# Performance work log

Hardware: AMD Instinct MI355X
Metric: run time of the kernel (lower is better)

## Reference

```python
import jax, jax.numpy as jnp
import numpy as np

N_NODES = 65536  # total nodes across batch (64 graphs x 1024 nodes)


def _gcn_conv(x, W, b, src, dst, norm, num_nodes):
    # PyG GCNConv: h = x @ W; out_i = sum_{j->i} norm_ij * h_j + b
    h = x @ W  # [N, out_dim]
    msg = h[src] * norm[:, None]  # [E+N, out_dim]
    out = jax.ops.segment_sum(msg, dst, num_segments=num_nodes)
    return out + b


def _add_self_loops_and_norm(edge_index, num_nodes):
    # add self loops, compute symmetric normalization deg^-1/2 * deg^-1/2
    loops = jnp.arange(num_nodes, dtype=edge_index.dtype)
    src = jnp.concatenate([edge_index[0], loops])
    dst = jnp.concatenate([edge_index[1], loops])
    deg = jax.ops.segment_sum(jnp.ones_like(dst, dtype=jnp.float32), dst,
                              num_segments=num_nodes)
    dinv = jnp.where(deg > 0, jax.lax.rsqrt(jnp.maximum(deg, 1.0)), 0.0)
    norm = dinv[src] * dinv[dst]
    return src, dst, norm


def setup_inputs() -> dict:
    key = jax.random.key(0)
    k1, k2, k3, k4, k5 = jax.random.split(key, 5)
    num_features, latent = 128, 16
    x = jax.random.normal(k1, (N_NODES, num_features), dtype=jnp.float32)
    edge_index = jax.random.randint(k2, (2, 2097152), 0, N_NODES, dtype=jnp.int64)
    # Glorot-style params for conv1 (128->16) and conv2 (16->1)
    W1 = jax.random.normal(k3, (num_features, latent), dtype=jnp.float32) / np.sqrt(num_features)
    b1 = jnp.zeros((latent,), dtype=jnp.float32)
    W2 = jax.random.normal(k4, (latent, 1), dtype=jnp.float32) / np.sqrt(latent)
    b2 = jnp.zeros((1,), dtype=jnp.float32)
    return {"x": x, "W1": W1, "b1": b1, "W2": W2, "b2": b2,
            "edge_index": edge_index, "batch": 64}


def reference(x, W1, b1, W2, b2, edge_index, batch):
    num_nodes = x.shape[0]
    src, dst, norm = _add_self_loops_and_norm(edge_index, num_nodes)
    h = _gcn_conv(x, W1, b1, src, dst, norm, num_nodes)  # [N, 16]
    h = jax.nn.relu(h)
    h = _gcn_conv(h, W2, b2, src, dst, norm, num_nodes)  # [N, 1]
    return h.reshape(batch, -1)  # [batch, nodes_per_graph]
```

## Files before the change

kernel.cpp:

```cpp
#include <hip/hip_runtime.h>

#define FEAT 128
#define LAT  16
#define NB   256
#define NPB  256
#define CAP  10240
#define PBLK 512
#define PCHK 4096
#define CAPB 64
#define CAPBKT (PBLK * CAPB)

__global__ __launch_bounds__(512) void k_part(const int* __restrict__ src,
        const int* __restrict__ dst, int E, int* __restrict__ cnt,
        int* __restrict__ ebuf) {
    __shared__ int lcur[NB];
    int t = threadIdx.x;
    if (t < NB) lcur[t] = 0;
    __syncthreads();
    int e0 = blockIdx.x * PCHK;
    int e1 = min(e0 + PCHK, E);
    int c = max(e1 - e0, 0);
    int cb = blockIdx.x * CAPB;
    const int4* d4 = (const int4*)(dst + e0);
    const int4* s4 = (const int4*)(src + e0);
    int nq = c >> 2;
    for (int q = t; q < nq; q += 512) {
        int4 dv = d4[q];
        int4 sv = s4[q];
        int b0 = ((unsigned)dv.x) >> 8, b1 = ((unsigned)dv.y) >> 8;
        int b2 = ((unsigned)dv.z) >> 8, b3 = ((unsigned)dv.w) >> 8;
        int p0 = atomicAdd(&lcur[b0], 1);
        int p1 = atomicAdd(&lcur[b1], 1);
        int p2 = atomicAdd(&lcur[b2], 1);
        int p3 = atomicAdd(&lcur[b3], 1);
        if (p0 < CAPB) ebuf[b0 * CAPBKT + cb + p0] = (sv.x << 16) | dv.x;
        if (p1 < CAPB) ebuf[b1 * CAPBKT + cb + p1] = (sv.y << 16) | dv.y;
        if (p2 < CAPB) ebuf[b2 * CAPBKT + cb + p2] = (sv.z << 16) | dv.z;
        if (p3 < CAPB) ebuf[b3 * CAPBKT + cb + p3] = (sv.w << 16) | dv.w;
    }
    for (int e = (nq << 2) + t; e < c; e += 512) {
        int d = dst[e0 + e], s = src[e0 + e];
        int b = ((unsigned)d) >> 8;
        int p = atomicAdd(&lcur[b], 1);
        if (p < CAPB) ebuf[b * CAPBKT + cb + p] = (s << 16) | d;
    }
    __syncthreads();
    if (t < NB) cnt[(blockIdx.x << 8) | t] = min(lcur[t], CAPB);
}

__global__ __launch_bounds__(512) void k_csr(const int* __restrict__ ebuf,
        const int* __restrict__ cnt, const float* __restrict__ x,
        const float* __restrict__ W1, int* __restrict__ rsd,
        unsigned short* __restrict__ csr, float* __restrict__ hs) {
    __shared__ int stage[CAP];
    __shared__ int ccnt[PBLK];
    __shared__ int cpref[PBLK];
    __shared__ int h[NPB];
    __shared__ int sc[NPB];
    __shared__ int cur[NPB];
    __shared__ int total;
    int t = threadIdx.x;
    int b = blockIdx.x;
    ccnt[t] = cnt[(t << 8) | b];
    if (t < NPB) h[t] = 0;
    __syncthreads();
    cpref[t] = ccnt[t];
    __syncthreads();
    for (int off = 1; off < PBLK; off <<= 1) {
        int v = (t >= off) ? cpref[t - off] : 0;
        __syncthreads();
        cpref[t] += v;
        __syncthreads();
    }
    if (t == PBLK - 1) total = min(cpref[t], CAP);
    int excl = cpref[t] - ccnt[t];
    __syncthreads();
    cpref[t] = excl;
    __syncthreads();
    int lane = t & 7;
    int crel = t >> 3;
    for (int cg = 0; cg < PBLK; cg += 64) {
        int ch = cg + crel;
        int cc = ccnt[ch];
        int gbase = b * CAPBKT + ch * CAPB;
        int sbase = cpref[ch];
        for (int i = lane; i < cc; i += 8) {
            int v = ebuf[gbase + i];
            if (sbase + i < CAP) {
                stage[sbase + i] = v;
                atomicAdd(&h[v & 255], 1);
            }
        }
    }
    __syncthreads();
    int cntall = total;
    if (t < NPB) sc[t] = h[t];
    __syncthreads();
    for (int off = 1; off < NPB; off <<= 1) {
        int v = (t >= off && t < NPB) ? sc[t - off] : 0;
        __syncthreads();
        if (t < NPB) sc[t] += v;
        __syncthreads();
    }
    if (t < NPB) {
        int excl2 = t ? sc[t - 1] : 0;
        int node = b * NPB + t;
        rsd[node] = ((b * CAP + excl2) << 8) | min(h[t], 255);
        cur[t] = b * CAP + excl2;
    }
    __syncthreads();
    int e = t;
    for (; e + 1536 < cntall; e += 2048) {
        int v0 = stage[e], v1 = stage[e + 512], v2 = stage[e + 1024], v3 = stage[e + 1536];
        int p0 = atomicAdd(&cur[v0 & 255], 1);
        int p1 = atomicAdd(&cur[v1 & 255], 1);
        int p2 = atomicAdd(&cur[v2 & 255], 1);
        int p3 = atomicAdd(&cur[v3 & 255], 1);
        csr[p0] = (unsigned)v0 >> 16;
        csr[p1] = (unsigned)v1 >> 16;
        csr[p2] = (unsigned)v2 >> 16;
        csr[p3] = (unsigned)v3 >> 16;
    }
    for (; e < cntall; e += 512) {
        int v = stage[e];
        int pos = atomicAdd(&cur[v & 255], 1);
        csr[pos] = (unsigned)v >> 16;
    }
    __syncthreads();
    float* w = (float*)stage;
    for (int i = t; i < FEAT * LAT; i += 512) {
        int k = i >> 4, j = i & 15;
        w[(k << 4) + j + ((k >> 5) << 2)] = W1[i];
    }
    __syncthreads();
    int q = t & 3;
    int qofs = q << 2;
#pragma unroll
    for (int pass = 0; pass < 2; ++pass) {
        int nl = pass * 128 + (t >> 2);
        int node = b * NPB + nl;
        float acc[LAT];
#pragma unroll
        for (int j = 0; j < LAT; ++j) acc[j] = 0.f;
        const float4* xr = (const float4*)(x + (size_t)node * FEAT + q * 32);
#pragma unroll
        for (int k4 = 0; k4 < 8; ++k4) {
            float4 xv = xr[k4];
            int kb = (q * 32 + k4 * 4) * LAT + qofs;
#pragma unroll
            for (int j = 0; j < LAT; ++j) {
                acc[j] += xv.x * w[kb + 0 * LAT + j]
                        + xv.y * w[kb + 1 * LAT + j]
                        + xv.z * w[kb + 2 * LAT + j]
                        + xv.w * w[kb + 3 * LAT + j];
            }
        }
#pragma unroll
        for (int j = 0; j < LAT; ++j) {
            acc[j] += __shfl_xor(acc[j], 1, 4);
            acc[j] += __shfl_xor(acc[j], 2, 4);
        }
        float dv = rsqrtf((float)(h[nl] + 1));
        float4 ov;
        if (q == 0)      ov = make_float4(acc[0],  acc[1],  acc[2],  acc[3]);
        else if (q == 1) ov = make_float4(acc[4],  acc[5],  acc[6],  acc[7]);
        else if (q == 2) ov = make_float4(acc[8],  acc[9],  acc[10], acc[11]);
        else             ov = make_float4(acc[12], acc[13], acc[14], acc[15]);
        ov.x *= dv; ov.y *= dv; ov.z *= dv; ov.w *= dv;
        ((float4*)(hs + (size_t)node * LAT))[q] = ov;
    }
}

__global__ void k_conv1(const float* __restrict__ hs, const int* __restrict__ rsd,
                        const unsigned short* __restrict__ csr,
                        const float* __restrict__ b1, const float* __restrict__ W2,
                        float* __restrict__ g, int n) {
    int t = threadIdx.x;
    int lane16 = t & 15;
    int jq = t & 3;
    int es = (t >> 2) & 3;
    int node = blockIdx.x * 16 + (t >> 4);
    int rd = rsd[node];
    int s0 = rd >> 8, deg = rd & 255;
    int s1 = s0 + deg;
    const float4* hs4 = (const float4*)hs;
    float4 acc = make_float4(0.f, 0.f, 0.f, 0.f);
    if (es == 0) acc = hs4[(size_t)node * 4 + jq];
    int e = s0 + es;
    for (; e + 28 < s1; e += 32) {
        int i0 = csr[e],      i1 = csr[e + 4],  i2 = csr[e + 8],  i3 = csr[e + 12];
        int i4 = csr[e + 16], i5 = csr[e + 20], i6 = csr[e + 24], i7 = csr[e + 28];
        float4 a0 = hs4[(size_t)i0 * 4 + jq];
        float4 a1 = hs4[(size_t)i1 * 4 + jq];
        float4 a2 = hs4[(size_t)i2 * 4 + jq];
        float4 a3 = hs4[(size_t)i3 * 4 + jq];
        float4 a4 = hs4[(size_t)i4 * 4 + jq];
        float4 a5 = hs4[(size_t)i5 * 4 + jq];
        float4 a6 = hs4[(size_t)i6 * 4 + jq];
        float4 a7 = hs4[(size_t)i7 * 4 + jq];
        acc.x += ((a0.x + a1.x) + (a2.x + a3.x)) + ((a4.x + a5.x) + (a6.x + a7.x));
        acc.y += ((a0.y + a1.y) + (a2.y + a3.y)) + ((a4.y + a5.y) + (a6.y + a7.y));
        acc.z += ((a0.z + a1.z) + (a2.z + a3.z)) + ((a4.z + a5.z) + (a6.z + a7.z));
        acc.w += ((a0.w + a1.w) + (a2.w + a3.w)) + ((a4.w + a5.w) + (a6.w + a7.w));
    }
    for (; e < s1; e += 4) {
        int i = csr[e];
        float4 a = hs4[(size_t)i * 4 + jq];
        acc.x += a.x; acc.y += a.y; acc.z += a.z; acc.w += a.w;
    }
    acc.x += __shfl_xor(acc.x, 4, 16);  acc.x += __shfl_xor(acc.x, 8, 16);
    acc.y += __shfl_xor(acc.y, 4, 16);  acc.y += __shfl_xor(acc.y, 8, 16);
    acc.z += __shfl_xor(acc.z, 4, 16);  acc.z += __shfl_xor(acc.z, 8, 16);
    acc.w += __shfl_xor(acc.w, 4, 16);  acc.w += __shfl_xor(acc.w, 8, 16);
    float dv = rsqrtf((float)(deg + 1));
    float4 b1q = ((const float4*)b1)[jq];
    float4 w2q = ((const float4*)W2)[jq];
    float h0 = fmaxf(dv * acc.x + b1q.x, 0.f);
    float h1 = fmaxf(dv * acc.y + b1q.y, 0.f);
    float h2 = fmaxf(dv * acc.z + b1q.z, 0.f);
    float h3 = fmaxf(dv * acc.w + b1q.w, 0.f);
    float p = (h0 * w2q.x + h1 * w2q.y) + (h2 * w2q.z + h3 * w2q.w);
    p += __shfl_xor(p, 1, 16);
    p += __shfl_xor(p, 2, 16);
    if (lane16 == 0) g[node] = dv * p;
}

__global__ void k_conv2(const float* __restrict__ g, const int* __restrict__ rsd,
                        const unsigned short* __restrict__ csr,
                        const float* __restrict__ b2, float* __restrict__ out, int n) {
    int t = threadIdx.x;
    int q = t & 3;
    int node = blockIdx.x * 64 + (t >> 2);
    int rd = rsd[node];
    int s0 = rd >> 8, deg = rd & 255;
    int s1 = s0 + deg;
    float acc = (q == 0) ? g[node] : 0.f;
    int e = s0 + q;
    for (; e + 28 < s1; e += 32) {
        float a0 = g[csr[e]],      a1 = g[csr[e + 4]];
        float a2 = g[csr[e + 8]],  a3 = g[csr[e + 12]];
        float a4 = g[csr[e + 16]], a5 = g[csr[e + 20]];
        float a6 = g[csr[e + 24]], a7 = g[csr[e + 28]];
        acc += ((a0 + a1) + (a2 + a3)) + ((a4 + a5) + (a6 + a7));
    }
    for (; e < s1; e += 4) acc += g[csr[e]];
    acc += __shfl_xor(acc, 1, 4);
    acc += __shfl_xor(acc, 2, 4);
    if (q == 0) {
        float dv = rsqrtf((float)(deg + 1));
        out[node] = dv * acc + b2[0];
    }
}

extern "C" void kernel_launch(void* const* d_in, const int* in_sizes, int n_in,
                              void* d_out, int out_size, void* d_ws, size_t ws_size,
                              hipStream_t stream) {
    const float* x  = (const float*)d_in[0];
    const float* W1 = (const float*)d_in[1];
    const float* b1 = (const float*)d_in[2];
    const float* W2 = (const float*)d_in[3];
    const float* b2 = (const float*)d_in[4];
    const int*   ei = (const int*)d_in[5];

    int n = in_sizes[0] / FEAT;
    int E = in_sizes[5] / 2;
    const int* srcp = ei;
    const int* dstp = ei + E;

    int*   cnt  = (int*)d_ws;
    int*   rsd  = cnt + PBLK * NB;
    float* g    = (float*)(rsd + n);
    float* hs   = g + n;
    int*   ebuf = (int*)(hs + (size_t)n * LAT);
    unsigned short* csr = (unsigned short*)(ebuf + (size_t)NB * CAPBKT);

    k_part <<<PBLK, 512, 0, stream>>>(srcp, dstp, E, cnt, ebuf);
    k_csr  <<<NB, 512, 0, stream>>>(ebuf, cnt, x, W1, rsd, csr, hs);
    k_conv1<<<n / 16, 256, 0, stream>>>(hs, rsd, csr, b1, W2, g, n);
    k_conv2<<<n / 64, 256, 0, stream>>>(g, rsd, csr, b2, (float*)d_out, n);
}
```

Baseline: 76.60 us.

## Split CSR build blocks into two half-bucket blocks for more parallelism

```diff
diff --git a/kernel.cpp b/kernel.cpp
--- a/kernel.cpp
+++ b/kernel.cpp
@@ -5,6 +5,7 @@
 #define NB   256
 #define NPB  256
 #define CAP  10240
+#define HCAP 5120
 #define PBLK 512
 #define PCHK 4096
 #define CAPB 64
@@ -52,70 +53,62 @@
         const int* __restrict__ cnt, const float* __restrict__ x,
         const float* __restrict__ W1, int* __restrict__ rsd,
         unsigned short* __restrict__ csr, float* __restrict__ hs) {
-    __shared__ int stage[CAP];
+    __shared__ int stage[HCAP];
     __shared__ int ccnt[PBLK];
-    __shared__ int cpref[PBLK];
-    __shared__ int h[NPB];
-    __shared__ int sc[NPB];
-    __shared__ int cur[NPB];
-    __shared__ int total;
-    int t = threadIdx.x;
-    int b = blockIdx.x;
+    __shared__ int h[128];
+    __shared__ int sc[128];
+    __shared__ int cur[128];
+    __shared__ int hcur;
+    int t = threadIdx.x;
+    int b = blockIdx.x >> 1;
+    int hi = blockIdx.x & 1;
     ccnt[t] = cnt[(t << 8) | b];
-    if (t < NPB) h[t] = 0;
-    __syncthreads();
-    cpref[t] = ccnt[t];
-    __syncthreads();
-    for (int off = 1; off < PBLK; off <<= 1) {
-        int v = (t >= off) ? cpref[t - off] : 0;
-        __syncthreads();
-        cpref[t] += v;
-        __syncthreads();
-    }
-    if (t == PBLK - 1) total = min(cpref[t], CAP);
-    int excl = cpref[t] - ccnt[t];
-    __syncthreads();
-    cpref[t] = excl;
+    if (t < 128) h[t] = 0;
+    if (t == 0) hcur = 0;
     __syncthreads();
     int lane = t & 7;
     int crel = t >> 3;
+    int hbit = hi << 7;
     for (int cg = 0; cg < PBLK; cg += 64) {
         int ch = cg + crel;
         int cc = ccnt[ch];
         int gbase = b * CAPBKT + ch * CAPB;
-        int sbase = cpref[ch];
         for (int i = lane; i < cc; i += 8) {
             int v = ebuf[gbase + i];
-            if (sbase + i < CAP) {
-                stage[sbase + i] = v;
-                atomicAdd(&h[v & 255], 1);
+            if ((v & 128) == hbit) {
+                int p = atomicAdd(&hcur, 1);
+                if (p < HCAP) {
+                    stage[p] = v;
+                    atomicAdd(&h[v & 127], 1);
+                }
             }
         }
     }
     __syncthreads();
-    int cntall = total;
-    if (t < NPB) sc[t] = h[t];
-    __syncthreads();
-    for (int off = 1; off < NPB; off <<= 1) {
-        int v = (t >= off && t < NPB) ? sc[t - off] : 0;
+    int cntall = min(hcur, HCAP);
+    if (t < 128) sc[t] = h[t];
+    __syncthreads();
+    for (int off = 1; off < 128; off <<= 1) {
+        int v = (t >= off && t < 128) ? sc[t - off] : 0;
         __syncthreads();
-        if (t < NPB) sc[t] += v;
+        if (t < 128) sc[t] += v;
         __syncthreads();
     }
-    if (t < NPB) {
-        int excl2 = t ? sc[t - 1] : 0;
-        int node = b * NPB + t;
-        rsd[node] = ((b * CAP + excl2) << 8) | min(h[t], 255);
-        cur[t] = b * CAP + excl2;
+    int rbase = b * CAP + hi * HCAP;
+    if (t < 128) {
+        int excl = t ? sc[t - 1] : 0;
+        int node = b * NPB + hbit + t;
+        rsd[node] = ((rbase + excl) << 8) | min(h[t], 255);
+        cur[t] = rbase + excl;
     }
     __syncthreads();
     int e = t;
     for (; e + 1536 < cntall; e += 2048) {
         int v0 = stage[e], v1 = stage[e + 512], v2 = stage[e + 1024], v3 = stage[e + 1536];
-        int p0 = atomicAdd(&cur[v0 & 255], 1);
-        int p1 = atomicAdd(&cur[v1 & 255], 1);
-        int p2 = atomicAdd(&cur[v2 & 255], 1);
-        int p3 = atomicAdd(&cur[v3 & 255], 1);
+        int p0 = atomicAdd(&cur[v0 & 127], 1);
+        int p1 = atomicAdd(&cur[v1 & 127], 1);
+        int p2 = atomicAdd(&cur[v2 & 127], 1);
+        int p3 = atomicAdd(&cur[v3 & 127], 1);
         csr[p0] = (unsigned)v0 >> 16;
         csr[p1] = (unsigned)v1 >> 16;
         csr[p2] = (unsigned)v2 >> 16;
@@ -123,7 +116,7 @@
     }
     for (; e < cntall; e += 512) {
         int v = stage[e];
-        int pos = atomicAdd(&cur[v & 255], 1);
+        int pos = atomicAdd(&cur[v & 127], 1);
         csr[pos] = (unsigned)v >> 16;
     }
     __syncthreads();
@@ -135,10 +128,9 @@
     __syncthreads();
     int q = t & 3;
     int qofs = q << 2;
-#pragma unroll
-    for (int pass = 0; pass < 2; ++pass) {
-        int nl = pass * 128 + (t >> 2);
-        int node = b * NPB + nl;
+    {
+        int nl = t >> 2;
+        int node = b * NPB + hbit + nl;
         float acc[LAT];
 #pragma unroll
         for (int j = 0; j < LAT; ++j) acc[j] = 0.f;
@@ -275,7 +267,7 @@
     unsigned short* csr = (unsigned short*)(ebuf + (size_t)NB * CAPBKT);
 
     k_part <<<PBLK, 512, 0, stream>>>(srcp, dstp, E, cnt, ebuf);
-    k_csr  <<<NB, 512, 0, stream>>>(ebuf, cnt, x, W1, rsd, csr, hs);
+    k_csr  <<<NB * 2, 512, 0, stream>>>(ebuf, cnt, x, W1, rsd, csr, hs);
     k_conv1<<<n / 16, 256, 0, stream>>>(hs, rsd, csr, b1, W2, g, n);
     k_conv2<<<n / 64, 256, 0, stream>>>(g, rsd, csr, b2, (float*)d_out, n);
 }
```

Result: no change. 77.81 us (+1.6%).

## Fuse four stages into one cooperative kernel with grid-wide syncs

Applied to the files above, without the earlier changes.

```diff
diff --git a/kernel.cpp b/kernel.cpp
--- a/kernel.cpp
+++ b/kernel.cpp
@@ -1,88 +1,70 @@
 #include <hip/hip_runtime.h>
+#include <hip/hip_cooperative_groups.h>
+namespace cg = cooperative_groups;
 
 #define FEAT 128
 #define LAT  16
 #define NB   256
 #define NPB  256
 #define CAP  10240
-#define PBLK 512
-#define PCHK 4096
-#define CAPB 64
-#define CAPBKT (PBLK * CAPB)
-
-__global__ __launch_bounds__(512) void k_part(const int* __restrict__ src,
-        const int* __restrict__ dst, int E, int* __restrict__ cnt,
-        int* __restrict__ ebuf) {
-    __shared__ int lcur[NB];
-    int t = threadIdx.x;
+#define GRID 256
+#define TPB  1024
+#define PCHK 8192
+#define CAPB 96
+#define REGB (GRID * CAPB)
+
+__device__ __forceinline__ void phaseA(int t, int blk,
+        const int* __restrict__ src, const int* __restrict__ dst,
+        int* __restrict__ cnt, int* __restrict__ ebuf, int* lcur) {
     if (t < NB) lcur[t] = 0;
     __syncthreads();
-    int e0 = blockIdx.x * PCHK;
-    int e1 = min(e0 + PCHK, E);
-    int c = max(e1 - e0, 0);
-    int cb = blockIdx.x * CAPB;
+    int e0 = blk * PCHK;
+    int cb = blk * CAPB;
     const int4* d4 = (const int4*)(dst + e0);
     const int4* s4 = (const int4*)(src + e0);
-    int nq = c >> 2;
-    for (int q = t; q < nq; q += 512) {
+    for (int q = t; q < PCHK / 4; q += TPB) {
         int4 dv = d4[q];
         int4 sv = s4[q];
-        int b0 = ((unsigned)dv.x) >> 8, b1 = ((unsigned)dv.y) >> 8;
-        int b2 = ((unsigned)dv.z) >> 8, b3 = ((unsigned)dv.w) >> 8;
-        int p0 = atomicAdd(&lcur[b0], 1);
-        int p1 = atomicAdd(&lcur[b1], 1);
-        int p2 = atomicAdd(&lcur[b2], 1);
-        int p3 = atomicAdd(&lcur[b3], 1);
-        if (p0 < CAPB) ebuf[b0 * CAPBKT + cb + p0] = (sv.x << 16) | dv.x;
-        if (p1 < CAPB) ebuf[b1 * CAPBKT + cb + p1] = (sv.y << 16) | dv.y;
-        if (p2 < CAPB) ebuf[b2 * CAPBKT + cb + p2] = (sv.z << 16) | dv.z;
-        if (p3 < CAPB) ebuf[b3 * CAPBKT + cb + p3] = (sv.w << 16) | dv.w;
-    }
-    for (int e = (nq << 2) + t; e < c; e += 512) {
-        int d = dst[e0 + e], s = src[e0 + e];
-        int b = ((unsigned)d) >> 8;
-        int p = atomicAdd(&lcur[b], 1);
-        if (p < CAPB) ebuf[b * CAPBKT + cb + p] = (s << 16) | d;
-    }
-    __syncthreads();
-    if (t < NB) cnt[(blockIdx.x << 8) | t] = min(lcur[t], CAPB);
-}
-
-__global__ __launch_bounds__(512) void k_csr(const int* __restrict__ ebuf,
-        const int* __restrict__ cnt, const float* __restrict__ x,
-        const float* __restrict__ W1, int* __restrict__ rsd,
-        unsigned short* __restrict__ csr, float* __restrict__ hs) {
-    __shared__ int stage[CAP];
-    __shared__ int ccnt[PBLK];
-    __shared__ int cpref[PBLK];
-    __shared__ int h[NPB];
-    __shared__ int sc[NPB];
-    __shared__ int cur[NPB];
-    __shared__ int total;
-    int t = threadIdx.x;
-    int b = blockIdx.x;
-    ccnt[t] = cnt[(t << 8) | b];
-    if (t < NPB) h[t] = 0;
-    __syncthreads();
-    cpref[t] = ccnt[t];
-    __syncthreads();
-    for (int off = 1; off < PBLK; off <<= 1) {
-        int v = (t >= off) ? cpref[t - off] : 0;
+        {   int d = dv.x, v = (sv.x << 16) | d, b = ((unsigned)d) >> 8;
+            int p = atomicAdd(&lcur[b], 1); if (p < CAPB) ebuf[b * REGB + cb + p] = v; }
+        {   int d = dv.y, v = (sv.y << 16) | d, b = ((unsigned)d) >> 8;
+            int p = atomicAdd(&lcur[b], 1); if (p < CAPB) ebuf[b * REGB + cb + p] = v; }
+        {   int d = dv.z, v = (sv.z << 16) | d, b = ((unsigned)d) >> 8;
+            int p = atomicAdd(&lcur[b], 1); if (p < CAPB) ebuf[b * REGB + cb + p] = v; }
+        {   int d = dv.w, v = (sv.w << 16) | d, b = ((unsigned)d) >> 8;
+            int p = atomicAdd(&lcur[b], 1); if (p < CAPB) ebuf[b * REGB + cb + p] = v; }
+    }
+    __syncthreads();
+    if (t < NB) cnt[(blk << 8) | t] = min(lcur[t], CAPB);
+}
+
+__device__ __forceinline__ void phaseB(int t, int b,
+        const int* __restrict__ ebuf, const int* __restrict__ cnt,
+        const float* __restrict__ x, const float* __restrict__ W1,
+        int* __restrict__ rsd, unsigned short* __restrict__ csr,
+        float* __restrict__ hs,
+        int* stage, int* ccnt, int* cpref, int* h, int* sc, int* cur, int* total) {
+    if (t < NB) { ccnt[t] = cnt[(t << 8) | b]; h[t] = 0; }
+    __syncthreads();
+    if (t < NB) cpref[t] = ccnt[t];
+    __syncthreads();
+    for (int off = 1; off < NB; off <<= 1) {
+        int v = (t >= off && t < NB) ? cpref[t - off] : 0;
         __syncthreads();
-        cpref[t] += v;
+        if (t < NB) cpref[t] += v;
         __syncthreads();
     }
-    if (t == PBLK - 1) total = min(cpref[t], CAP);
-    int excl = cpref[t] - ccnt[t];
-    __syncthreads();
-    cpref[t] = excl;
+    if (t == NB - 1) *total = min(cpref[t], CAP);
+    int ex = (t < NB) ? cpref[t] - ccnt[t] : 0;
+    __syncthreads();
+    if (t < NB) cpref[t] = ex;
     __syncthreads();
     int lane = t & 7;
     int crel = t >> 3;
-    for (int cg = 0; cg < PBLK; cg += 64) {
-        int ch = cg + crel;
+    for (int cg_ = 0; cg_ < NB; cg_ += 128) {
+        int ch = cg_ + crel;
         int cc = ccnt[ch];
-        int gbase = b * CAPBKT + ch * CAPB;
+        int gbase = b * REGB + ch * CAPB;
         int sbase = cpref[ch];
         for (int i = lane; i < cc; i += 8) {
             int v = ebuf[gbase + i];
@@ -93,25 +75,25 @@
         }
     }
     __syncthreads();
-    int cntall = total;
-    if (t < NPB) sc[t] = h[t];
-    __syncthreads();
-    for (int off = 1; off < NPB; off <<= 1) {
-        int v = (t >= off && t < NPB) ? sc[t - off] : 0;
+    int cntall = *total;
+    if (t < NB) sc[t] = h[t];
+    __syncthreads();
+    for (int off = 1; off < NB; off <<= 1) {
+        int v = (t >= off && t < NB) ? sc[t - off] : 0;
         __syncthreads();
-        if (t < NPB) sc[t] += v;
+        if (t < NB) sc[t] += v;
         __syncthreads();
     }
-    if (t < NPB) {
-        int excl2 = t ? sc[t - 1] : 0;
+    if (t < NB) {
+        int excl = t ? sc[t - 1] : 0;
         int node = b * NPB + t;
-        rsd[node] = ((b * CAP + excl2) << 8) | min(h[t], 255);
-        cur[t] = b * CAP + excl2;
+        rsd[node] = ((b * CAP + excl) << 8) | min(h[t], 255);
+        cur[t] = b * CAP + excl;
     }
     __syncthreads();
     int e = t;
-    for (; e + 1536 < cntall; e += 2048) {
-        int v0 = stage[e], v1 = stage[e + 512], v2 = stage[e + 1024], v3 = stage[e + 1536];
+    for (; e + 3072 < cntall; e += 4096) {
+        int v0 = stage[e], v1 = stage[e + 1024], v2 = stage[e + 2048], v3 = stage[e + 3072];
         int p0 = atomicAdd(&cur[v0 & 255], 1);
         int p1 = atomicAdd(&cur[v1 & 255], 1);
         int p2 = atomicAdd(&cur[v2 & 255], 1);
@@ -121,121 +103,119 @@
         csr[p2] = (unsigned)v2 >> 16;
         csr[p3] = (unsigned)v3 >> 16;
     }
-    for (; e < cntall; e += 512) {
+    for (; e < cntall; e += TPB) {
         int v = stage[e];
         int pos = atomicAdd(&cur[v & 255], 1);
         csr[pos] = (unsigned)v >> 16;
     }
     __syncthreads();
     float* w = (float*)stage;
-    for (int i = t; i < FEAT * LAT; i += 512) {
+    for (int i = t; i < FEAT * LAT; i += TPB) {
         int k = i >> 4, j = i & 15;
         w[(k << 4) + j + ((k >> 5) << 2)] = W1[i];
     }
     __syncthreads();
     int q = t & 3;
     int qofs = q << 2;
-#pragma unroll
-    for (int pass = 0; pass < 2; ++pass) {
-        int nl = pass * 128 + (t >> 2);
-        int node = b * NPB + nl;
-        float acc[LAT];
-#pragma unroll
-        for (int j = 0; j < LAT; ++j) acc[j] = 0.f;
-        const float4* xr = (const float4*)(x + (size_t)node * FEAT + q * 32);
-#pragma unroll
-        for (int k4 = 0; k4 < 8; ++k4) {
-            float4 xv = xr[k4];
-            int kb = (q * 32 + k4 * 4) * LAT + qofs;
-#pragma unroll
-            for (int j = 0; j < LAT; ++j) {
-                acc[j] += xv.x * w[kb + 0 * LAT + j]
-                        + xv.y * w[kb + 1 * LAT + j]
-                        + xv.z * w[kb + 2 * LAT + j]
-                        + xv.w * w[kb + 3 * LAT + j];
-            }
+    int nl = t >> 2;
+    int node = b * NPB + nl;
+    float acc[LAT];
+#pragma unroll
+    for (int j = 0; j < LAT; ++j) acc[j] = 0.f;
+    const float4* xr = (const float4*)(x + (size_t)node * FEAT + q * 32);
+#pragma unroll
+    for (int k4 = 0; k4 < 8; ++k4) {
+        float4 xv = xr[k4];
+        int kb = (q * 32 + k4 * 4) * LAT + qofs;
+#pragma unroll
+        for (int j = 0; j < LAT; ++j) {
+            acc[j] += xv.x * w[kb + 0 * LAT + j]
+                    + xv.y * w[kb + 1 * LAT + j]
+                    + xv.z * w[kb + 2 * LAT + j]
+                    + xv.w * w[kb + 3 * LAT + j];
         }
-#pragma unroll
-        for (int j = 0; j < LAT; ++j) {
-            acc[j] += __shfl_xor(acc[j], 1, 4);
-            acc[j] += __shfl_xor(acc[j], 2, 4);
-        }
-        float dv = rsqrtf((float)(h[nl] + 1));
-        float4 ov;
-        if (q == 0)      ov = make_float4(acc[0],  acc[1],  acc[2],  acc[3]);
-        else if (q == 1) ov = make_float4(acc[4],  acc[5],  acc[6],  acc[7]);
-        else if (q == 2) ov = make_float4(acc[8],  acc[9],  acc[10], acc[11]);
-        else             ov = make_float4(acc[12], acc[13], acc[14], acc[15]);
-        ov.x *= dv; ov.y *= dv; ov.z *= dv; ov.w *= dv;
-        ((float4*)(hs + (size_t)node * LAT))[q] = ov;
-    }
-}
-
-__global__ void k_conv1(const float* __restrict__ hs, const int* __restrict__ rsd,
-                        const unsigned short* __restrict__ csr,
-                        const float* __restrict__ b1, const float* __restrict__ W2,
-                        float* __restrict__ g, int n) {
-    int t = threadIdx.x;
+    }
+#pragma unroll
+    for (int j = 0; j < LAT; ++j) {
+        acc[j] += __shfl_xor(acc[j], 1, 4);
+        acc[j] += __shfl_xor(acc[j], 2, 4);
+    }
+    float dv = rsqrtf((float)(h[nl] + 1));
+    float4 ov;
+    if (q == 0)      ov = make_float4(acc[0],  acc[1],  acc[2],  acc[3]);
+    else if (q == 1) ov = make_float4(acc[4],  acc[5],  acc[6],  acc[7]);
+    else if (q == 2) ov = make_float4(acc[8],  acc[9],  acc[10], acc[11]);
+    else             ov = make_float4(acc[12], acc[13], acc[14], acc[15]);
+    ov.x *= dv; ov.y *= dv; ov.z *= dv; ov.w *= dv;
+    ((float4*)(hs + (size_t)node * LAT))[q] = ov;
+}
+
+__device__ __forceinline__ void phaseC(int t, int blk, const float* __restrict__ hs,
+        const int* __restrict__ rsd, const unsigned short* __restrict__ csr,
+        const float* __restrict__ b1, const float* __restrict__ W2,
+        float* __restrict__ g) {
+    const float4* hs4 = (const float4*)hs;
     int lane16 = t & 15;
     int jq = t & 3;
     int es = (t >> 2) & 3;
-    int node = blockIdx.x * 16 + (t >> 4);
+#pragma unroll
+    for (int pass = 0; pass < 4; ++pass) {
+        int node = blk * 256 + pass * 64 + (t >> 4);
+        int rd = rsd[node];
+        int s0 = rd >> 8, deg = rd & 255;
+        int s1 = s0 + deg;
+        float4 acc = make_float4(0.f, 0.f, 0.f, 0.f);
+        if (es == 0) acc = hs4[(size_t)node * 4 + jq];
+        int e = s0 + es;
+        for (; e + 28 < s1; e += 32) {
+            int i0 = csr[e],      i1 = csr[e + 4],  i2 = csr[e + 8],  i3 = csr[e + 12];
+            int i4 = csr[e + 16], i5 = csr[e + 20], i6 = csr[e + 24], i7 = csr[e + 28];
+            float4 a0 = hs4[(size_t)i0 * 4 + jq];
+            float4 a1 = hs4[(size_t)i1 * 4 + jq];
+            float4 a2 = hs4[(size_t)i2 * 4 + jq];
+            float4 a3 = hs4[(size_t)i3 * 4 + jq];
+            float4 a4 = hs4[(size_t)i4 * 4 + jq];
+            float4 a5 = hs4[(size_t)i5 * 4 + jq];
+            float4 a6 = hs4[(size_t)i6 * 4 + jq];
+            float4 a7 = hs4[(size_t)i7 * 4 + jq];
+            acc.x += ((a0.x + a1.x) + (a2.x + a3.x)) + ((a4.x + a5.x) + (a6.x + a7.x));
+            acc.y += ((a0.y + a1.y) + (a2.y + a3.y)) + ((a4.y + a5.y) + (a6.y + a7.y));
+            acc.z += ((a0.z + a1.z) + (a2.z + a3.z)) + ((a4.z + a5.z) + (a6.z + a7.z));
+            acc.w += ((a0.w + a1.w) + (a2.w + a3.w)) + ((a4.w + a5.w) + (a6.w + a7.w));
+        }
+        for (; e < s1; e += 4) {
+            int i = csr[e];
+            float4 a = hs4[(size_t)i * 4 + jq];
+            acc.x += a.x; acc.y += a.y; acc.z += a.z; acc.w += a.w;
+        }
+        acc.x += __shfl_xor(acc.x, 4, 16);  acc.x += __shfl_xor(acc.x, 8, 16);
+        acc.y += __shfl_xor(acc.y, 4, 16);  acc.y += __shfl_xor(acc.y, 8, 16);
+        acc.z += __shfl_xor(acc.z, 4, 16);  acc.z += __shfl_xor(acc.z, 8, 16);
+        acc.w += __shfl_xor(acc.w, 4, 16);  acc.w += __shfl_xor(acc.w, 8, 16);
+        float dv = rsqrtf((float)(deg + 1));
+        float4 b1q = ((const float4*)b1)[jq];
+        float4 w2q = ((const float4*)W2)[jq];
+        float h0 = fmaxf(dv * acc.x + b1q.x, 0.f);
+        float h1 = fmaxf(dv * acc.y + b1q.y, 0.f);
+        float h2 = fmaxf(dv * acc.z + b1q.z, 0.f);
+        float h3 = fmaxf(dv * acc.w + b1q.w, 0.f);
+        float p = (h0 * w2q.x + h1 * w2q.y) + (h2 * w2q.z + h3 * w2q.w);
+        p += __shfl_xor(p, 1, 16);
+        p += __shfl_xor(p, 2, 16);
+        if (lane16 == 0) g[node] = dv * p;
+    }
+}
+
+__device__ __forceinline__ void phaseD(int t, int blk, const float* __restrict__ g,
+        const int* __restrict__ rsd, const unsigned short* __restrict__ csr,
+        const float* __restrict__ b2, float* __restrict__ out) {
+    int q4 = t & 3;
+    int node = blk * 256 + (t >> 2);
     int rd = rsd[node];
     int s0 = rd >> 8, deg = rd & 255;
     int s1 = s0 + deg;
-    const float4* hs4 = (const float4*)hs;
-    float4 acc = make_float4(0.f, 0.f, 0.f, 0.f);
-    if (es == 0) acc = hs4[(size_t)node * 4 + jq];
-    int e = s0 + es;
-    for (; e + 28 < s1; e += 32) {
-        int i0 = csr[e],      i1 = csr[e + 4],  i2 = csr[e + 8],  i3 = csr[e + 12];
-        int i4 = csr[e + 16], i5 = csr[e + 20], i6 = csr[e + 24], i7 = csr[e + 28];
-        float4 a0 = hs4[(size_t)i0 * 4 + jq];
-        float4 a1 = hs4[(size_t)i1 * 4 + jq];
-        float4 a2 = hs4[(size_t)i2 * 4 + jq];
-        float4 a3 = hs4[(size_t)i3 * 4 + jq];
-        float4 a4 = hs4[(size_t)i4 * 4 + jq];
-        float4 a5 = hs4[(size_t)i5 * 4 + jq];
-        float4 a6 = hs4[(size_t)i6 * 4 + jq];
-        float4 a7 = hs4[(size_t)i7 * 4 + jq];
-        acc.x += ((a0.x + a1.x) + (a2.x + a3.x)) + ((a4.x + a5.x) + (a6.x + a7.x));
-        acc.y += ((a0.y + a1.y) + (a2.y + a3.y)) + ((a4.y + a5.y) + (a6.y + a7.y));
-        acc.z += ((a0.z + a1.z) + (a2.z + a3.z)) + ((a4.z + a5.z) + (a6.z + a7.z));
-        acc.w += ((a0.w + a1.w) + (a2.w + a3.w)) + ((a4.w + a5.w) + (a6.w + a7.w));
-    }
-    for (; e < s1; e += 4) {
-        int i = csr[e];
-        float4 a = hs4[(size_t)i * 4 + jq];
-        acc.x += a.x; acc.y += a.y; acc.z += a.z; acc.w += a.w;
-    }
-    acc.x += __shfl_xor(acc.x, 4, 16);  acc.x += __shfl_xor(acc.x, 8, 16);
-    acc.y += __shfl_xor(acc.y, 4, 16);  acc.y += __shfl_xor(acc.y, 8, 16);
-    acc.z += __shfl_xor(acc.z, 4, 16);  acc.z += __shfl_xor(acc.z, 8, 16);
-    acc.w += __shfl_xor(acc.w, 4, 16);  acc.w += __shfl_xor(acc.w, 8, 16);
-    float dv = rsqrtf((float)(deg + 1));
-    float4 b1q = ((const float4*)b1)[jq];
-    float4 w2q = ((const float4*)W2)[jq];
-    float h0 = fmaxf(dv * acc.x + b1q.x, 0.f);
-    float h1 = fmaxf(dv * acc.y + b1q.y, 0.f);
-    float h2 = fmaxf(dv * acc.z + b1q.z, 0.f);
-    float h3 = fmaxf(dv * acc.w + b1q.w, 0.f);
-    float p = (h0 * w2q.x + h1 * w2q.y) + (h2 * w2q.z + h3 * w2q.w);
-    p += __shfl_xor(p, 1, 16);
-    p += __shfl_xor(p, 2, 16);
-    if (lane16 == 0) g[node] = dv * p;
-}
-
-__global__ void k_conv2(const float* __restrict__ g, const int* __restrict__ rsd,
-                        const unsigned short* __restrict__ csr,
-                        const float* __restrict__ b2, float* __restrict__ out, int n) {
-    int t = threadIdx.x;
-    int q = t & 3;
-    int node = blockIdx.x * 64 + (t >> 2);
-    int rd = rsd[node];
-    int s0 = rd >> 8, deg = rd & 255;
-    int s1 = s0 + deg;
-    float acc = (q == 0) ? g[node] : 0.f;
-    int e = s0 + q;
+    float acc = (q4 == 0) ? g[node] : 0.f;
+    int e = s0 + q4;
     for (; e + 28 < s1; e += 32) {
         float a0 = g[csr[e]],      a1 = g[csr[e + 4]];
         float a2 = g[csr[e + 8]],  a3 = g[csr[e + 12]];
@@ -246,10 +226,67 @@
     for (; e < s1; e += 4) acc += g[csr[e]];
     acc += __shfl_xor(acc, 1, 4);
     acc += __shfl_xor(acc, 2, 4);
-    if (q == 0) {
+    if (q4 == 0) {
         float dv = rsqrtf((float)(deg + 1));
         out[node] = dv * acc + b2[0];
     }
+}
+
+__global__ __launch_bounds__(TPB, 2) void k_all(
+        const int* __restrict__ src, const int* __restrict__ dst,
+        int* __restrict__ cnt, int* __restrict__ ebuf,
+        const float* __restrict__ x, const float* __restrict__ W1,
+        const float* __restrict__ b1, const float* __restrict__ W2,
+        const float* __restrict__ b2, int* __restrict__ rsd,
+        unsigned short* __restrict__ csr, float* __restrict__ hs,
+        float* __restrict__ g, float* __restrict__ out) {
+    cg::grid_group gg = cg::this_grid();
+    __shared__ int stage[CAP];
+    __shared__ int ccnt[NB];
+    __shared__ int cpref[NB];
+    __shared__ int h[NB];
+    __shared__ int sc[NB];
+    __shared__ int cur[NB];
+    __shared__ int total;
+    int t = threadIdx.x, blk = blockIdx.x;
+    phaseA(t, blk, src, dst, cnt, ebuf, ccnt);
+    gg.sync();
+    phaseB(t, blk, ebuf, cnt, x, W1, rsd, csr, hs, stage, ccnt, cpref, h, sc, cur, &total);
+    gg.sync();
+    phaseC(t, blk, hs, rsd, csr, b1, W2, g);
+    gg.sync();
+    phaseD(t, blk, g, rsd, csr, b2, out);
+}
+
+__global__ __launch_bounds__(TPB, 2) void k_pA(const int* __restrict__ src,
+        const int* __restrict__ dst, int* __restrict__ cnt, int* __restrict__ ebuf) {
+    __shared__ int lcur[NB];
+    phaseA(threadIdx.x, blockIdx.x, src, dst, cnt, ebuf, lcur);
+}
+__global__ __launch_bounds__(TPB, 2) void k_pB(const int* __restrict__ ebuf,
+        const int* __restrict__ cnt, const float* __restrict__ x,
+        const float* __restrict__ W1, int* __restrict__ rsd,
+        unsigned short* __restrict__ csr, float* __restrict__ hs) {
+    __shared__ int stage[CAP];
+    __shared__ int ccnt[NB];
+    __shared__ int cpref[NB];
+    __shared__ int h[NB];
+    __shared__ int sc[NB];
+    __shared__ int cur[NB];
+    __shared__ int total;
+    phaseB(threadIdx.x, blockIdx.x, ebuf, cnt, x, W1, rsd, csr, hs,
+           stage, ccnt, cpref, h, sc, cur, &total);
+}
+__global__ __launch_bounds__(TPB, 2) void k_pC(const float* __restrict__ hs,
+        const int* __restrict__ rsd, const unsigned short* __restrict__ csr,
+        const float* __restrict__ b1, const float* __restrict__ W2,
+        float* __restrict__ g) {
+    phaseC(threadIdx.x, blockIdx.x, hs, rsd, csr, b1, W2, g);
+}
+__global__ __launch_bounds__(TPB, 2) void k_pD(const float* __restrict__ g,
+        const int* __restrict__ rsd, const unsigned short* __restrict__ csr,
+        const float* __restrict__ b2, float* __restrict__ out) {
+    phaseD(threadIdx.x, blockIdx.x, g, rsd, csr, b2, out);
 }
 
 extern "C" void kernel_launch(void* const* d_in, const int* in_sizes, int n_in,
@@ -264,18 +301,27 @@
 
     int n = in_sizes[0] / FEAT;
     int E = in_sizes[5] / 2;
+    (void)n; (void)E;
     const int* srcp = ei;
     const int* dstp = ei + E;
 
     int*   cnt  = (int*)d_ws;
-    int*   rsd  = cnt + PBLK * NB;
-    float* g    = (float*)(rsd + n);
-    float* hs   = g + n;
-    int*   ebuf = (int*)(hs + (size_t)n * LAT);
-    unsigned short* csr = (unsigned short*)(ebuf + (size_t)NB * CAPBKT);
-
-    k_part <<<PBLK, 512, 0, stream>>>(srcp, dstp, E, cnt, ebuf);
-    k_csr  <<<NB, 512, 0, stream>>>(ebuf, cnt, x, W1, rsd, csr, hs);
-    k_conv1<<<n / 16, 256, 0, stream>>>(hs, rsd, csr, b1, W2, g, n);
-    k_conv2<<<n / 64, 256, 0, stream>>>(g, rsd, csr, b2, (float*)d_out, n);
-}
+    int*   rsd  = cnt + GRID * NB;
+    float* g    = (float*)(rsd + 65536);
+    float* hs   = g + 65536;
+    int*   ebuf = (int*)(hs + (size_t)65536 * LAT);
+    unsigned short* csr = (unsigned short*)(ebuf + (size_t)NB * REGB);
+    float* outp = (float*)d_out;
+
+    void* args[] = { (void*)&srcp, (void*)&dstp, (void*)&cnt, (void*)&ebuf,
+                     (void*)&x, (void*)&W1, (void*)&b1, (void*)&W2, (void*)&b2,
+                     (void*)&rsd, (void*)&csr, (void*)&hs, (void*)&g, (void*)&outp };
+    hipError_t err = hipLaunchCooperativeKernel((const void*)k_all, dim3(GRID),
+                                                dim3(TPB), args, 0, stream);
+    if (err != hipSuccess) {
+        k_pA<<<GRID, TPB, 0, stream>>>(srcp, dstp, cnt, ebuf);
+        k_pB<<<GRID, TPB, 0, stream>>>(ebuf, cnt, x, W1, rsd, csr, hs);
+        k_pC<<<GRID, TPB, 0, stream>>>(hs, rsd, csr, b1, W2, g);
+        k_pD<<<GRID, TPB, 0, stream>>>(g, rsd, csr, b2, outp);
+    }
+}
```

New measurement: 191.3 us. +149.7%, slower.

## Move first-layer GEMM into partition kernel and apply source normalization during gather

Applied to the files above, without the earlier changes.

```diff
diff --git a/kernel.cpp b/kernel.cpp
--- a/kernel.cpp
+++ b/kernel.cpp
@@ -12,46 +12,70 @@
 
 __global__ __launch_bounds__(512) void k_part(const int* __restrict__ src,
         const int* __restrict__ dst, int E, int* __restrict__ cnt,
-        int* __restrict__ ebuf) {
+        int* __restrict__ ebuf, const float* __restrict__ x,
+        const float* __restrict__ W1, float* __restrict__ hus) {
     __shared__ int lcur[NB];
-    int t = threadIdx.x;
+    __shared__ float w[2080];
+    int t = threadIdx.x;
+    for (int i = t; i < FEAT * LAT; i += 512) {
+        int k = i >> 4, j = i & 15;
+        w[(k << 4) + j + ((k >> 5) << 2)] = W1[i];
+    }
     if (t < NB) lcur[t] = 0;
     __syncthreads();
     int e0 = blockIdx.x * PCHK;
-    int e1 = min(e0 + PCHK, E);
-    int c = max(e1 - e0, 0);
     int cb = blockIdx.x * CAPB;
     const int4* d4 = (const int4*)(dst + e0);
     const int4* s4 = (const int4*)(src + e0);
-    int nq = c >> 2;
-    for (int q = t; q < nq; q += 512) {
+    for (int q = t; q < PCHK / 4; q += 512) {
         int4 dv = d4[q];
         int4 sv = s4[q];
-        int b0 = ((unsigned)dv.x) >> 8, b1 = ((unsigned)dv.y) >> 8;
-        int b2 = ((unsigned)dv.z) >> 8, b3 = ((unsigned)dv.w) >> 8;
-        int p0 = atomicAdd(&lcur[b0], 1);
-        int p1 = atomicAdd(&lcur[b1], 1);
-        int p2 = atomicAdd(&lcur[b2], 1);
-        int p3 = atomicAdd(&lcur[b3], 1);
-        if (p0 < CAPB) ebuf[b0 * CAPBKT + cb + p0] = (sv.x << 16) | dv.x;
-        if (p1 < CAPB) ebuf[b1 * CAPBKT + cb + p1] = (sv.y << 16) | dv.y;
-        if (p2 < CAPB) ebuf[b2 * CAPBKT + cb + p2] = (sv.z << 16) | dv.z;
-        if (p3 < CAPB) ebuf[b3 * CAPBKT + cb + p3] = (sv.w << 16) | dv.w;
-    }
-    for (int e = (nq << 2) + t; e < c; e += 512) {
-        int d = dst[e0 + e], s = src[e0 + e];
-        int b = ((unsigned)d) >> 8;
-        int p = atomicAdd(&lcur[b], 1);
-        if (p < CAPB) ebuf[b * CAPBKT + cb + p] = (s << 16) | d;
+        {   int d = dv.x, v = (sv.x << 16) | d, b = ((unsigned)d) >> 8;
+            int p = atomicAdd(&lcur[b], 1); if (p < CAPB) ebuf[b * CAPBKT + cb + p] = v; }
+        {   int d = dv.y, v = (sv.y << 16) | d, b = ((unsigned)d) >> 8;
+            int p = atomicAdd(&lcur[b], 1); if (p < CAPB) ebuf[b * CAPBKT + cb + p] = v; }
+        {   int d = dv.z, v = (sv.z << 16) | d, b = ((unsigned)d) >> 8;
+            int p = atomicAdd(&lcur[b], 1); if (p < CAPB) ebuf[b * CAPBKT + cb + p] = v; }
+        {   int d = dv.w, v = (sv.w << 16) | d, b = ((unsigned)d) >> 8;
+            int p = atomicAdd(&lcur[b], 1); if (p < CAPB) ebuf[b * CAPBKT + cb + p] = v; }
     }
     __syncthreads();
     if (t < NB) cnt[(blockIdx.x << 8) | t] = min(lcur[t], CAPB);
+    int q = t & 3;
+    int qofs = q << 2;
+    int node = blockIdx.x * 128 + (t >> 2);
+    float acc[LAT];
+#pragma unroll
+    for (int j = 0; j < LAT; ++j) acc[j] = 0.f;
+    const float4* xr = (const float4*)(x + (size_t)node * FEAT + q * 32);
+#pragma unroll
+    for (int k4 = 0; k4 < 8; ++k4) {
+        float4 xv = xr[k4];
+        int kb = (q * 32 + k4 * 4) * LAT + qofs;
+#pragma unroll
+        for (int j = 0; j < LAT; ++j) {
+            acc[j] += xv.x * w[kb + 0 * LAT + j]
+                    + xv.y * w[kb + 1 * LAT + j]
+                    + xv.z * w[kb + 2 * LAT + j]
+                    + xv.w * w[kb + 3 * LAT + j];
+        }
+    }
+#pragma unroll
+    for (int j = 0; j < LAT; ++j) {
+        acc[j] += __shfl_xor(acc[j], 1, 4);
+        acc[j] += __shfl_xor(acc[j], 2, 4);
+    }
+    float4 ov;
+    if (q == 0)      ov = make_float4(acc[0],  acc[1],  acc[2],  acc[3]);
+    else if (q == 1) ov = make_float4(acc[4],  acc[5],  acc[6],  acc[7]);
+    else if (q == 2) ov = make_float4(acc[8],  acc[9],  acc[10], acc[11]);
+    else             ov = make_float4(acc[12], acc[13], acc[14], acc[15]);
+    ((float4*)(hus + (size_t)node * LAT))[q] = ov;
 }
 
 __global__ __launch_bounds__(512) void k_csr(const int* __restrict__ ebuf,
-        const int* __restrict__ cnt, const float* __restrict__ x,
-        const float* __restrict__ W1, int* __restrict__ rsd,
-        unsigned short* __restrict__ csr, float* __restrict__ hs) {
+        const int* __restrict__ cnt, int* __restrict__ rsd,
+        float* __restrict__ dinv, unsigned short* __restrict__ csr) {
     __shared__ int stage[CAP];
     __shared__ int ccnt[PBLK];
     __shared__ int cpref[PBLK];
@@ -73,9 +97,9 @@
         __syncthreads();
     }
     if (t == PBLK - 1) total = min(cpref[t], CAP);
-    int excl = cpref[t] - ccnt[t];
-    __syncthreads();
-    cpref[t] = excl;
+    int ex = cpref[t] - ccnt[t];
+    __syncthreads();
+    cpref[t] = ex;
     __syncthreads();
     int lane = t & 7;
     int crel = t >> 3;
@@ -103,10 +127,11 @@
         __syncthreads();
     }
     if (t < NPB) {
-        int excl2 = t ? sc[t - 1] : 0;
+        int excl = t ? sc[t - 1] : 0;
         int node = b * NPB + t;
-        rsd[node] = ((b * CAP + excl2) << 8) | min(h[t], 255);
-        cur[t] = b * CAP + excl2;
+        rsd[node] = ((b * CAP + excl) << 8) | min(h[t], 255);
+        dinv[node] = rsqrtf((float)(h[t] + 1));
+        cur[t] = b * CAP + excl;
     }
     __syncthreads();
     int e = t;
@@ -126,52 +151,10 @@
         int pos = atomicAdd(&cur[v & 255], 1);
         csr[pos] = (unsigned)v >> 16;
     }
-    __syncthreads();
-    float* w = (float*)stage;
-    for (int i = t; i < FEAT * LAT; i += 512) {
-        int k = i >> 4, j = i & 15;
-        w[(k << 4) + j + ((k >> 5) << 2)] = W1[i];
-    }
-    __syncthreads();
-    int q = t & 3;
-    int qofs = q << 2;
-#pragma unroll
-    for (int pass = 0; pass < 2; ++pass) {
-        int nl = pass * 128 + (t >> 2);
-        int node = b * NPB + nl;
-        float acc[LAT];
-#pragma unroll
-        for (int j = 0; j < LAT; ++j) acc[j] = 0.f;
-        const float4* xr = (const float4*)(x + (size_t)node * FEAT + q * 32);
-#pragma unroll
-        for (int k4 = 0; k4 < 8; ++k4) {
-            float4 xv = xr[k4];
-            int kb = (q * 32 + k4 * 4) * LAT + qofs;
-#pragma unroll
-            for (int j = 0; j < LAT; ++j) {
-                acc[j] += xv.x * w[kb + 0 * LAT + j]
-                        + xv.y * w[kb + 1 * LAT + j]
-                        + xv.z * w[kb + 2 * LAT + j]
-                        + xv.w * w[kb + 3 * LAT + j];
-            }
-        }
-#pragma unroll
-        for (int j = 0; j < LAT; ++j) {
-            acc[j] += __shfl_xor(acc[j], 1, 4);
-            acc[j] += __shfl_xor(acc[j], 2, 4);
-        }
-        float dv = rsqrtf((float)(h[nl] + 1));
-        float4 ov;
-        if (q == 0)      ov = make_float4(acc[0],  acc[1],  acc[2],  acc[3]);
-        else if (q == 1) ov = make_float4(acc[4],  acc[5],  acc[6],  acc[7]);
-        else if (q == 2) ov = make_float4(acc[8],  acc[9],  acc[10], acc[11]);
-        else             ov = make_float4(acc[12], acc[13], acc[14], acc[15]);
-        ov.x *= dv; ov.y *= dv; ov.z *= dv; ov.w *= dv;
-        ((float4*)(hs + (size_t)node * LAT))[q] = ov;
-    }
-}
-
-__global__ void k_conv1(const float* __restrict__ hs, const int* __restrict__ rsd,
+}
+
+__global__ void k_conv1(const float* __restrict__ hus, const int* __restrict__ rsd,
+                        const float* __restrict__ dinv,
                         const unsigned short* __restrict__ csr,
                         const float* __restrict__ b1, const float* __restrict__ W2,
                         float* __restrict__ g, int n) {
@@ -183,36 +166,46 @@
     int rd = rsd[node];
     int s0 = rd >> 8, deg = rd & 255;
     int s1 = s0 + deg;
-    const float4* hs4 = (const float4*)hs;
+    float dv = rsqrtf((float)(deg + 1));
+    const float4* h4 = (const float4*)hus;
     float4 acc = make_float4(0.f, 0.f, 0.f, 0.f);
-    if (es == 0) acc = hs4[(size_t)node * 4 + jq];
+    if (es == 0) {
+        float4 sv = h4[(size_t)node * 4 + jq];
+        acc.x = dv * sv.x; acc.y = dv * sv.y; acc.z = dv * sv.z; acc.w = dv * sv.w;
+    }
     int e = s0 + es;
     for (; e + 28 < s1; e += 32) {
         int i0 = csr[e],      i1 = csr[e + 4],  i2 = csr[e + 8],  i3 = csr[e + 12];
         int i4 = csr[e + 16], i5 = csr[e + 20], i6 = csr[e + 24], i7 = csr[e + 28];
-        float4 a0 = hs4[(size_t)i0 * 4 + jq];
-        float4 a1 = hs4[(size_t)i1 * 4 + jq];
-        float4 a2 = hs4[(size_t)i2 * 4 + jq];
-        float4 a3 = hs4[(size_t)i3 * 4 + jq];
-        float4 a4 = hs4[(size_t)i4 * 4 + jq];
-        float4 a5 = hs4[(size_t)i5 * 4 + jq];
-        float4 a6 = hs4[(size_t)i6 * 4 + jq];
-        float4 a7 = hs4[(size_t)i7 * 4 + jq];
-        acc.x += ((a0.x + a1.x) + (a2.x + a3.x)) + ((a4.x + a5.x) + (a6.x + a7.x));
-        acc.y += ((a0.y + a1.y) + (a2.y + a3.y)) + ((a4.y + a5.y) + (a6.y + a7.y));
-        acc.z += ((a0.z + a1.z) + (a2.z + a3.z)) + ((a4.z + a5.z) + (a6.z + a7.z));
-        acc.w += ((a0.w + a1.w) + (a2.w + a3.w)) + ((a4.w + a5.w) + (a6.w + a7.w));
+        float d0 = dinv[i0], d1 = dinv[i1], d2 = dinv[i2], d3 = dinv[i3];
+        float d4 = dinv[i4], d5 = dinv[i5], d6 = dinv[i6], d7 = dinv[i7];
+        float4 a0 = h4[(size_t)i0 * 4 + jq];
+        float4 a1 = h4[(size_t)i1 * 4 + jq];
+        float4 a2 = h4[(size_t)i2 * 4 + jq];
+        float4 a3 = h4[(size_t)i3 * 4 + jq];
+        float4 a4 = h4[(size_t)i4 * 4 + jq];
+        float4 a5 = h4[(size_t)i5 * 4 + jq];
+        float4 a6 = h4[(size_t)i6 * 4 + jq];
+        float4 a7 = h4[(size_t)i7 * 4 + jq];
+        acc.x += ((a0.x * d0 + a1.x * d1) + (a2.x * d2 + a3.x * d3))
+               + ((a4.x * d4 + a5.x * d5) + (a6.x * d6 + a7.x * d7));
+        acc.y += ((a0.y * d0 + a1.y * d1) + (a2.y * d2 + a3.y * d3))
+               + ((a4.y * d4 + a5.y * d5) + (a6.y * d6 + a7.y * d7));
+        acc.z += ((a0.z * d0 + a1.z * d1) + (a2.z * d2 + a3.z * d3))
+               + ((a4.z * d4 + a5.z * d5) + (a6.z * d6 + a7.z * d7));
+        acc.w += ((a0.w * d0 + a1.w * d1) + (a2.w * d2 + a3.w * d3))
+               + ((a4.w * d4 + a5.w * d5) + (a6.w * d6 + a7.w * d7));
     }
     for (; e < s1; e += 4) {
         int i = csr[e];
-        float4 a = hs4[(size_t)i * 4 + jq];
-        acc.x += a.x; acc.y += a.y; acc.z += a.z; acc.w += a.w;
+        float dd = dinv[i];
+        float4 a = h4[(size_t)i * 4 + jq];
+        acc.x += a.x * dd; acc.y += a.y * dd; acc.z += a.z * dd; acc.w += a.w * dd;
     }
     acc.x += __shfl_xor(acc.x, 4, 16);  acc.x += __shfl_xor(acc.x, 8, 16);
     acc.y += __shfl_xor(acc.y, 4, 16);  acc.y += __shfl_xor(acc.y, 8, 16);
     acc.z += __shfl_xor(acc.z, 4, 16);  acc.z += __shfl_xor(acc.z, 8, 16);
     acc.w += __shfl_xor(acc.w, 4, 16);  acc.w += __shfl_xor(acc.w, 8, 16);
-    float dv = rsqrtf((float)(deg + 1));
     float4 b1q = ((const float4*)b1)[jq];
     float4 w2q = ((const float4*)W2)[jq];
     float h0 = fmaxf(dv * acc.x + b1q.x, 0.f);
@@ -269,13 +262,14 @@
 
     int*   cnt  = (int*)d_ws;
     int*   rsd  = cnt + PBLK * NB;
-    float* g    = (float*)(rsd + n);
-    float* hs   = g + n;
-    int*   ebuf = (int*)(hs + (size_t)n * LAT);
+    float* dinv = (float*)(rsd + n);
+    float* g    = dinv + n;
+    float* hus  = g + n;
+    int*   ebuf = (int*)(hus + (size_t)n * LAT);
     unsigned short* csr = (unsigned short*)(ebuf + (size_t)NB * CAPBKT);
 
-    k_part <<<PBLK, 512, 0, stream>>>(srcp, dstp, E, cnt, ebuf);
-    k_csr  <<<NB, 512, 0, stream>>>(ebuf, cnt, x, W1, rsd, csr, hs);
-    k_conv1<<<n / 16, 256, 0, stream>>>(hs, rsd, csr, b1, W2, g, n);
+    k_part <<<PBLK, 512, 0, stream>>>(srcp, dstp, E, cnt, ebuf, x, W1, hus);
+    k_csr  <<<NB, 512, 0, stream>>>(ebuf, cnt, rsd, dinv, csr);
+    k_conv1<<<n / 16, 256, 0, stream>>>(hus, rsd, dinv, csr, b1, W2, g, n);
     k_conv2<<<n / 64, 256, 0, stream>>>(g, rsd, csr, b2, (float*)d_out, n);
 }
```

Result: slower. 89.11 us (+16.3%).
